# Optimization experiments

Hardware: AMD Instinct MI355X
Metric: run time of the kernel (lower is better)

Reference implementation:

```python
import jax, jax.numpy as jnp
import numpy as np

N = 16      # hparams.length (utterances)
T = 128     # tokens per utterance
D = 256     # local_feature_dim
DG = 256    # global_attention.input_dim
ATT = 128   # attention inner dim
R1 = 2 * N * N  # rgcn num_relations
H1 = 256    # rgcn.dim
H2 = 256    # gcn.dim
NEG = -1e9


def setup_inputs() -> dict:
    ks = jax.random.split(jax.random.key(0), 16)
    s = 0.02
    return {
        "global_features": jax.random.normal(ks[0], (N, DG), jnp.float32),
        "local_features": jax.random.normal(ks[1], (N, T, D), jnp.float32),
        "speaker": jax.random.randint(ks[2], (N,), 0, 2),
        "length": jax.random.randint(ks[3], (N,), 1, T + 1),
        # Bahdanau global attention params
        "Wq": jax.random.normal(ks[4], (DG, ATT), jnp.float32) * s,
        "Wk": jax.random.normal(ks[5], (DG, ATT), jnp.float32) * s,
        "v_att": jax.random.normal(ks[6], (ATT,), jnp.float32) * s,
        # Bidirectional local attention params
        "Wb1": jax.random.normal(ks[7], (D, ATT), jnp.float32) * s,
        "Wb2": jax.random.normal(ks[8], (D, ATT), jnp.float32) * s,
        # RGCN layer 1 (2*N^2 relations)
        "Wrel1": jax.random.normal(ks[9], (R1, D, H1), jnp.float32) * s,
        "Wroot1": jax.random.normal(ks[10], (D, H1), jnp.float32) * s,
        "b1": jnp.zeros((H1,), jnp.float32),
        # RGCN layer 2 (1 relation)
        "Wrel2": jax.random.normal(ks[11], (1, H1, H2), jnp.float32) * s,
        "Wroot2": jax.random.normal(ks[12], (H1, H2), jnp.float32) * s,
        "b2": jnp.zeros((H2,), jnp.float32),
    }


def _rgcn_fg(x, Wrel, Wroot, b, e_src, e_dst, rel, ew, n_nodes):
    # x: [N,T,din], ew: [E,Ts,Td] (src-token x dst-token weights), Wrel: [R,din,dout]
    We = Wrel[rel]                 # [E,din,dout] irregular gather over relations
    xs = x[e_src]                  # [E,T,din]
    # message aligned with dst tokens: sum over src tokens t -> dst token s
    msg = jnp.einsum('ets,etd,edo->eso', ew, xs, We)   # [E,T,dout]
    agg = jax.ops.segment_sum(msg, e_dst, num_segments=n_nodes)
    return agg + x @ Wroot + b


def reference(global_features, local_features, speaker, length,
              Wq, Wk, v_att, Wb1, Wb2,
              Wrel1, Wroot1, b1, Wrel2, Wroot2, b2):
    n = global_features.shape[0]
    t = local_features.shape[1]

    # --- Bahdanau global attention: query i over keys j ---
    q = global_features @ Wq                         # [N,A]
    k = global_features @ Wk                         # [N,A]
    s = jnp.tanh(q[:, None, :] + k[None, :, :]) @ v_att   # [N,N]
    gw = jax.nn.softmax(s, axis=1).reshape(-1)       # [N*N]

    # --- Bidirectional local attention, vectorized over all (i,j) pairs ---
    p1 = local_features @ Wb1                        # [N,T,A]
    p2 = local_features @ Wb2                        # [N,T,A]
    S = jnp.einsum('ita,jsa->ijts', p1, p2)          # [N,N,T,T]
    pos = jnp.arange(t)
    valid = pos[None, :] < length[:, None]           # [N,T]
    S = jnp.where(valid[None, :, None, :], S, NEG)   # mask key tokens of j
    w1 = jax.nn.softmax(S, axis=-1)                  # softmax over j's tokens
    w1 = w1 * valid[:, None, :, None]                # zero padded query rows of i
    lw = w1.reshape(n * n, t, t)                     # [E,T,T]

    # --- edge weights & relation ids ---
    ew1 = gw[:, None, None] * lw                     # [E,T,T]
    e_src = jnp.arange(n * n) // n                   # edge (i,j): src=i
    e_dst = jnp.arange(n * n) % n                    # dst=j
    direction = jnp.where(e_src < e_dst, 0, 1)
    rel = (speaker[e_src] * n + speaker[e_dst]) * 2 + direction

    # --- two attention-weighted relational GCN layers ---
    x1 = _rgcn_fg(local_features, Wrel1, Wroot1, b1, e_src, e_dst, rel, ew1, n)
    x2 = _rgcn_fg(x1, Wrel2, Wroot2, b2, e_src, e_dst, jnp.zeros_like(rel), lw, n)
    return x2
```

## Files before the change

### kernel.cpp

```cpp
#include <hip/hip_runtime.h>

#define NODES 16
#define TT    128
#define DIM   256
#define ATTD  128
#define HD    256
#define NEGV  -1e9f

typedef short bf16x8 __attribute__((ext_vector_type(8)));
typedef float f32x4  __attribute__((ext_vector_type(4)));
typedef unsigned short ushort_t;
typedef ushort_t u16x4 __attribute__((ext_vector_type(4)));
typedef ushort_t u16x8 __attribute__((ext_vector_type(8)));

__device__ __forceinline__ ushort_t f2b(float f) {
  union { float f; unsigned u; } v; v.f = f;
  unsigned r = (v.u + 0x7fffu + ((v.u >> 16) & 1u)) >> 16;
  return (ushort_t)r;
}
__device__ __forceinline__ float b2f(ushort_t h) {
  union { unsigned u; float f; } v; v.u = ((unsigned)h) << 16; return v.f;
}

__device__ __forceinline__ void wave_gemm_step(const ushort_t* __restrict__ A, int as, int R0,
                                               const ushort_t* __restrict__ BT, int bs, int C0,
                                               int kb, int lr, f32x4 acc[4][4]) {
  bf16x8 a[4], b[4];
#pragma unroll
  for (int m = 0; m < 4; ++m)
    a[m] = *(const bf16x8*)(A + (size_t)(R0 + m * 16 + lr) * as + kb);
#pragma unroll
  for (int n = 0; n < 4; ++n)
    b[n] = *(const bf16x8*)(BT + (size_t)(C0 + n * 16 + lr) * bs + kb);
#pragma unroll
  for (int m = 0; m < 4; ++m)
#pragma unroll
    for (int n = 0; n < 4; ++n)
      acc[m][n] = __builtin_amdgcn_mfma_f32_16x16x32_bf16(a[m], b[n], acc[m][n], 0, 0, 0);
}

#define WAVE_SETUP                                    \
  int tid = threadIdx.x;                              \
  int wave = tid >> 6, lane = tid & 63;               \
  int wr = wave >> 1, wc = wave & 1;                  \
  int lr = lane & 15, kg = lane >> 4;                 \
  (void)wr; (void)wc;

#define ACC_INIT(acc)                                 \
  f32x4 acc[4][4];                                    \
  { f32x4 z = {0.f, 0.f, 0.f, 0.f};                   \
    _Pragma("unroll") for (int m = 0; m < 4; ++m)     \
    _Pragma("unroll") for (int n = 0; n < 4; ++n) acc[m][n] = z; }

__device__ __forceinline__ void stage_half(const ushort_t* __restrict__ src, int srcs,
                                           ushort_t* __restrict__ dst, int tid) {
#pragma unroll
  for (int p = 0; p < 4; ++p) {
    int idx = p * 256 + tid;
    int row = idx >> 3;
    int cb  = (idx & 7) << 4;
    u16x8 v = *(const u16x8*)(src + (size_t)row * srcs + (cb >> 1));
    *(u16x8*)((char*)dst + row * 128 + (cb ^ ((row & 7) << 4))) = v;
  }
}

__device__ __forceinline__ void gemm_half(const ushort_t* __restrict__ bufA,
                                          const ushort_t* __restrict__ bufB,
                                          int R0, int C0, int lr, int kg,
                                          f32x4 acc[4][4]) {
#pragma unroll
  for (int kk = 0; kk < 2; ++kk) {
    int cb = kk * 64 + kg * 16;
    bf16x8 a[4], b[4];
#pragma unroll
    for (int m = 0; m < 4; ++m) {
      int row = R0 + m * 16 + lr;
      a[m] = *(const bf16x8*)((const char*)bufA + row * 128 + (cb ^ ((row & 7) << 4)));
    }
#pragma unroll
    for (int n = 0; n < 4; ++n) {
      int row = C0 + n * 16 + lr;
      b[n] = *(const bf16x8*)((const char*)bufB + row * 128 + (cb ^ ((row & 7) << 4)));
    }
#pragma unroll
    for (int m = 0; m < 4; ++m)
#pragma unroll
      for (int n = 0; n < 4; ++n)
        acc[m][n] = __builtin_amdgcn_mfma_f32_16x16x32_bf16(a[m], b[n], acc[m][n], 0, 0, 0);
  }
}

__global__ void k_prep(const float* __restrict__ Lf, ushort_t* __restrict__ Lfh,
                       const float* __restrict__ Wb1, const float* __restrict__ Wb2,
                       const float* __restrict__ Wroot1, const float* __restrict__ Wroot2,
                       const float* __restrict__ Wrel2, const float* __restrict__ Wrel1,
                       ushort_t* __restrict__ Wb1T, ushort_t* __restrict__ Wb2T,
                       ushort_t* __restrict__ Wroot1T, ushort_t* __restrict__ Wroot2T,
                       ushort_t* __restrict__ Wrel2T, ushort_t* __restrict__ Wrel1T8,
                       const float* __restrict__ G, const float* __restrict__ Wq,
                       const float* __restrict__ Wk, float* __restrict__ qk) {
  int blk = blockIdx.x;
  if (blk < 256) {
    int gi = blk * 256 + threadIdx.x;
    const float4* src = (const float4*)Lf;
    float4 v0 = src[gi * 2], v1 = src[gi * 2 + 1];
    u16x8 o;
    o[0] = f2b(v0.x); o[1] = f2b(v0.y); o[2] = f2b(v0.z); o[3] = f2b(v0.w);
    o[4] = f2b(v1.x); o[5] = f2b(v1.y); o[6] = f2b(v1.z); o[7] = f2b(v1.w);
    *(u16x8*)(Lfh + (size_t)gi * 8) = o;
  } else if (blk < 448) {
    __shared__ float lds[64][65];
    int b = blk - 256;
    const float* src; ushort_t* dst; int C, t;
    if (b < 8)       { src = Wb1;    dst = Wb1T;    C = 128; t = b; }
    else if (b < 16) { src = Wb2;    dst = Wb2T;    C = 128; t = b - 8; }
    else if (b < 32) { src = Wroot1; dst = Wroot1T; C = 256; t = b - 16; }
    else if (b < 48) { src = Wroot2; dst = Wroot2T; C = 256; t = b - 32; }
    else if (b < 64) { src = Wrel2;  dst = Wrel2T;  C = 256; t = b - 48; }
    else {
      int m = (b - 64) >> 4;
      int relid = (m >> 2) * 32 + (m & 3);
      src = Wrel1 + (size_t)relid * 65536;
      dst = Wrel1T8 + (size_t)m * 65536;
      C = 256; t = (b - 64) & 15;
    }
    int tilesC = C >> 6;
    int r0 = (t / tilesC) * 64, c0 = (t % tilesC) * 64;
    int tid = threadIdx.x;
    for (int p = 0; p < 16; ++p) {
      int idx = p * 256 + tid, rr = idx >> 6, cc = idx & 63;
      lds[rr][cc] = src[(size_t)(r0 + rr) * C + c0 + cc];
    }
    __syncthreads();
    for (int p = 0; p < 16; ++p) {
      int idx = p * 256 + tid, rr = idx >> 6, cc = idx & 63;
      dst[(size_t)(c0 + rr) * 256 + r0 + cc] = f2b(lds[cc][rr]);
    }
  } else {
    int i = blk - 448, t = threadIdx.x;
    const float* W = (t < 128) ? Wq : Wk;
    int a = t & 127;
    float acc = 0.f;
#pragma unroll 8
    for (int d = 0; d < DIM; ++d)
      acc = fmaf(G[i * DIM + d], W[d * ATTD + a], acc);
    int dst = (t < 128) ? i : (NODES + i);
    qk[(size_t)dst * ATTD + a] = acc;
  }
}

__global__ __launch_bounds__(256, 1)
void k_phaseB(const float* __restrict__ qk, const float* __restrict__ vatt,
              float* __restrict__ gw,
              const ushort_t* __restrict__ Lfh,
              const ushort_t* __restrict__ Wb1T, const ushort_t* __restrict__ Wb2T,
              ushort_t* __restrict__ p1h, ushort_t* __restrict__ p2h,
              const ushort_t* __restrict__ Wroot1T, const float* __restrict__ b1,
              float* __restrict__ x1part,
              const ushort_t* __restrict__ Wrel1T8, const int* __restrict__ spk,
              ushort_t* __restrict__ YT) {
  __shared__ union {
    ushort_t buf[2][16384];
    struct { float sred[NODES][17]; float q[ATTD]; } sc;
  } sh;
  int blk = blockIdx.x;
  if (blk < 16) {
    int i = blk, t = threadIdx.x;
    int j = t >> 4, ag = t & 15;
    if (t < ATTD) sh.sc.q[t] = qk[(size_t)i * ATTD + t];
    __syncthreads();
    float sum = 0.f;
#pragma unroll
    for (int u = 0; u < 8; ++u) {
      int a = ag * 8 + u;
      sum += tanhf(sh.sc.q[a] + qk[(size_t)(NODES + j) * ATTD + a]) * vatt[a];
    }
    sh.sc.sred[j][ag] = sum;
    __syncthreads();
    if (t < NODES) {
      float s = 0.f;
#pragma unroll
      for (int u = 0; u < 16; ++u) s += sh.sc.sred[t][u];
      sh.sc.sred[t][16] = s;
    }
    __syncthreads();
    if (t == 0) {
      float m = -1e30f;
      for (int jj = 0; jj < NODES; ++jj) m = fmaxf(m, sh.sc.sred[jj][16]);
      float ex[NODES], ssum = 0.f;
      for (int jj = 0; jj < NODES; ++jj) { ex[jj] = __expf(sh.sc.sred[jj][16] - m); ssum += ex[jj]; }
      float inv = 1.f / ssum;
      for (int jj = 0; jj < NODES; ++jj) gw[i * NODES + jj] = ex[jj] * inv;
    }
    return;
  }
  WAVE_SETUP
  const ushort_t* Asrc; const ushort_t* Bsrc;
  if (blk < 48) {
    int t = blk - 16; int sel = t >> 4, bx = t & 15;
    Asrc = Lfh + (size_t)bx * 128 * DIM;
    Bsrc = sel ? Wb2T : Wb1T;
  } else if (blk < 80) {
    int t = blk - 48; int bx = t & 15, by = t >> 4;
    Asrc = Lfh + (size_t)bx * 128 * DIM;
    Bsrc = Wroot1T + (size_t)by * 128 * DIM;
  } else {
    int t = blk - 80; int iq = t >> 1, cy = t & 1;
    int i = iq >> 2, q = iq & 3;
    int m8 = spk[i] * 4 + q;
    Asrc = Lfh + (size_t)i * TT * DIM;
    Bsrc = Wrel1T8 + (size_t)m8 * 65536 + (size_t)cy * 128 * DIM;
  }
  stage_half(Asrc, DIM, sh.buf[0], tid);
  stage_half(Bsrc, DIM, sh.buf[0] + 8192, tid);
  __syncthreads();
  ACC_INIT(acc)
  for (int c = 1; c < 4; ++c) {
    stage_half(Asrc + c * 64, DIM, sh.buf[c & 1], tid);
    stage_half(Bsrc + c * 64, DIM, sh.buf[c & 1] + 8192, tid);
    gemm_half(sh.buf[(c & 1) ^ 1], sh.buf[(c & 1) ^ 1] + 8192, wr * 64, wc * 64, lr, kg, acc);
    __syncthreads();
  }
  gemm_half(sh.buf[1], sh.buf[1] + 8192, wr * 64, wc * 64, lr, kg, acc);
  if (blk < 48) {
    int t = blk - 16; int sel = t >> 4, bx = t & 15;
    ushort_t* out = sel ? p2h : p1h;
    int R0 = bx * 128 + wr * 64, C0 = wc * 64;
#pragma unroll
    for (int m = 0; m < 4; ++m)
#pragma unroll
      for (int n = 0; n < 4; ++n) {
        int col = C0 + n * 16 + lr;
#pragma unroll
        for (int r = 0; r < 4; ++r) {
          int row = R0 + m * 16 + kg * 4 + r;
          out[(size_t)row * ATTD + col] = f2b(acc[m][n][r]);
        }
      }
  } else if (blk < 80) {
    int t = blk - 48; int bx = t & 15, by = t >> 4;
    int R0 = bx * 128 + wr * 64, C0 = by * 128 + wc * 64;
#pragma unroll
    for (int m = 0; m < 4; ++m)
#pragma unroll
      for (int n = 0; n < 4; ++n) {
        int col = C0 + n * 16 + lr;
        float bb = b1[col];
#pragma unroll
        for (int r = 0; r < 4; ++r) {
          int row = R0 + m * 16 + kg * 4 + r;
          x1part[(size_t)row * HD + col] = acc[m][n][r] + bb;
        }
      }
  } else {
    int t = blk - 80; int iq = t >> 1, cy = t & 1;
    int R0 = wr * 64, C0 = cy * 128 + wc * 64;
#pragma unroll
    for (int m = 0; m < 4; ++m)
#pragma unroll
      for (int n = 0; n < 4; ++n) {
        int o = C0 + n * 16 + lr;
        int t0 = R0 + m * 16 + kg * 4;
        u16x4 v;
#pragma unroll
        for (int r = 0; r < 4; ++r) v[r] = f2b(acc[m][n][r]);
        *(u16x4*)(YT + (size_t)iq * 32768 + (size_t)o * TT + t0) = v;
      }
  }
}

__global__ __launch_bounds__(256, 1)
void k_locatt(const ushort_t* __restrict__ p1h, const ushort_t* __restrict__ p2h,
              const int* __restrict__ length,
              ushort_t* __restrict__ lwT) {
  __shared__ union {
    ushort_t buf[2][16384];
    float S[TT][129];
  } sh;
  __shared__ float red[TT][2];
  __shared__ float sInv[TT];
  int e = blockIdx.x, i = e >> 4, j = e & 15;
  WAVE_SETUP
  int R0 = wr * 64, C0 = wc * 64;
  const ushort_t* A = p1h + (size_t)i * TT * ATTD;
  const ushort_t* B = p2h + (size_t)j * TT * ATTD;
  stage_half(A, ATTD, sh.buf[0], tid);
  stage_half(B, ATTD, sh.buf[0] + 8192, tid);
  __syncthreads();
  stage_half(A + 64, ATTD, sh.buf[1], tid);
  stage_half(B + 64, ATTD, sh.buf[1] + 8192, tid);
  ACC_INIT(acc)
  gemm_half(sh.buf[0], sh.buf[0] + 8192, R0, C0, lr, kg, acc);
  __syncthreads();
  gemm_half(sh.buf[1], sh.buf[1] + 8192, R0, C0, lr, kg, acc);
  __syncthreads();
#pragma unroll
  for (int m = 0; m < 4; ++m)
#pragma unroll
    for (int n = 0; n < 4; ++n)
#pragma unroll
      for (int r = 0; r < 4; ++r)
        sh.S[R0 + m * 16 + kg * 4 + r][C0 + n * 16 + lr] = acc[m][n][r];
  __syncthreads();
  int leni = length[i], lenj = length[j];
  int t = tid & 127, h = tid >> 7, s0 = h * 64;
  float mx = -1e30f;
  for (int s = s0; s < s0 + 64; ++s) {
    float vv = (s < lenj) ? sh.S[t][s] : NEGV;
    mx = fmaxf(mx, vv);
  }
  red[t][h] = mx;
  __syncthreads();
  mx = fmaxf(red[t][0], red[t][1]);
  __syncthreads();
  float sum = 0.f;
  for (int s = s0; s < s0 + 64; ++s) {
    float vv = (s < lenj) ? sh.S[t][s] : NEGV;
    float ee = __expf(vv - mx);
    sh.S[t][s] = ee;
    sum += ee;
  }
  red[t][h] = sum;
  __syncthreads();
  if (h == 0) sInv[t] = (t < leni) ? 1.f / (red[t][0] + red[t][1]) : 0.f;
  __syncthreads();
  int s = tid >> 1;
  int t0 = (tid & 1) * 64;
  size_t base = (size_t)e * 16384 + (size_t)s * TT;
  for (int tb = 0; tb < 64; tb += 8) {
    u16x8 w;
#pragma unroll
    for (int u = 0; u < 8; ++u) {
      int tt = t0 + tb + u;
      w[u] = f2b(sh.S[tt][s] * sInv[tt]);
    }
    *(u16x8*)(lwT + base + t0 + tb) = w;
  }
}

__global__ __launch_bounds__(256, 1)
void k_wagg(const ushort_t* __restrict__ lwT, const ushort_t* __restrict__ Bsrc,
            const float* __restrict__ gw, const int* __restrict__ spk,
            ushort_t* __restrict__ partH, int mode) {
  __shared__ ushort_t buf[2][16384];
  int g = blockIdx.x, j = blockIdx.y, oh = blockIdx.z;
  WAVE_SETUP
  int R0 = wr * 64, C0 = wc * 64;
  int i0 = g * 2, i1 = g * 2 + 1;
  int e0 = i0 * NODES + j, e1 = i1 * NODES + j;
  const ushort_t* B0;
  const ushort_t* B1;
  float ge0, ge1;
  if (mode == 1) {
    int q0 = spk[j] * 2 + ((i0 < j) ? 0 : 1);
    int q1 = spk[j] * 2 + ((i1 < j) ? 0 : 1);
    B0 = Bsrc + (size_t)(i0 * 4 + q0) * 32768 + (size_t)oh * 16384;
    B1 = Bsrc + (size_t)(i1 * 4 + q1) * 32768 + (size_t)oh * 16384;
    ge0 = gw[e0]; ge1 = gw[e1];
  } else {
    B0 = Bsrc + (size_t)i0 * 32768 + (size_t)oh * 16384;
    B1 = Bsrc + (size_t)i1 * 32768 + (size_t)oh * 16384;
    ge0 = 1.f; ge1 = 1.f;
  }
  const ushort_t* A0 = lwT + (size_t)e0 * 16384;
  const ushort_t* A1 = lwT + (size_t)e1 * 16384;
  stage_half(A0, TT, buf[0], tid);
  stage_half(B0, TT, buf[0] + 8192, tid);
  __syncthreads();
  stage_half(A0 + 64, TT, buf[1], tid);
  stage_half(B0 + 64, TT, buf[1] + 8192, tid);
  ACC_INIT(acc0)
  gemm_half(buf[0], buf[0] + 8192, R0, C0, lr, kg, acc0);
  __syncthreads();
  stage_half(A1, TT, buf[0], tid);
  stage_half(B1, TT, buf[0] + 8192, tid);
  gemm_half(buf[1], buf[1] + 8192, R0, C0, lr, kg, acc0);
  __syncthreads();
  stage_half(A1 + 64, TT, buf[1], tid);
  stage_half(B1 + 64, TT, buf[1] + 8192, tid);
  ACC_INIT(acc1)
  gemm_half(buf[0], buf[0] + 8192, R0, C0, lr, kg, acc1);
  __syncthreads();
  gemm_half(buf[1], buf[1] + 8192, R0, C0, lr, kg, acc1);
  size_t base = (size_t)(g * NODES + j) * TT * HD + (size_t)oh * 128;
#pragma unroll
  for (int m = 0; m < 4; ++m)
#pragma unroll
    for (int n = 0; n < 4; ++n) {
      int ocol = C0 + n * 16 + lr;
#pragma unroll
      for (int r = 0; r < 4; ++r) {
        int s = R0 + m * 16 + kg * 4 + r;
        partH[base + (size_t)s * HD + ocol] = f2b(ge0 * acc0[m][n][r] + ge1 * acc1[m][n][r]);
      }
    }
}

__global__ __launch_bounds__(256, 1)
void k_reduce1(const ushort_t* __restrict__ partH, const float* __restrict__ x1part,
               ushort_t* __restrict__ x1h, ushort_t* __restrict__ x1T) {
  __shared__ ushort_t L[TT][40];
  int j = blockIdx.x, oc0 = blockIdx.y * 32, tid = threadIdx.x;
  const size_t Q = (size_t)NODES * TT * HD;
#pragma unroll
  for (int p = 0; p < 4; ++p) {
    int idx = p * 256 + tid;
    int t = idx >> 3, o4 = (idx & 7) * 4;
    size_t goff = ((size_t)j * TT + t) * HD + oc0 + o4;
    float4 s = *(const float4*)(x1part + goff);
#pragma unroll
    for (int g = 0; g < 8; ++g) {
      u16x4 pv = *(const u16x4*)(partH + (size_t)g * Q + goff);
      s.x += b2f(pv[0]); s.y += b2f(pv[1]); s.z += b2f(pv[2]); s.w += b2f(pv[3]);
    }
    u16x4 hv; hv[0] = f2b(s.x); hv[1] = f2b(s.y); hv[2] = f2b(s.z); hv[3] = f2b(s.w);
    *(u16x4*)(x1h + goff) = hv;
    *(u16x4*)(&L[t][o4]) = hv;
  }
  __syncthreads();
#pragma unroll
  for (int p = 0; p < 2; ++p) {
    int idx = p * 256 + tid;
    int o = idx >> 4, t8 = (idx & 15) * 8;
    u16x8 v;
#pragma unroll
    for (int u = 0; u < 8; ++u) v[u] = L[t8 + u][o];
    *(u16x8*)(x1T + (size_t)j * 32768 + (size_t)(oc0 + o) * TT + t8) = v;
  }
}

__global__ void k_reduce2(const ushort_t* __restrict__ partH, ushort_t* __restrict__ Z2h) {
  int idx = blockIdx.x * 256 + threadIdx.x;
  size_t o4 = (size_t)idx * 4;
  const size_t Q = (size_t)NODES * TT * HD;
  float4 s = {0.f, 0.f, 0.f, 0.f};
#pragma unroll
  for (int g = 0; g < 8; ++g) {
    u16x4 pv = *(const u16x4*)(partH + (size_t)g * Q + o4);
    s.x += b2f(pv[0]); s.y += b2f(pv[1]); s.z += b2f(pv[2]); s.w += b2f(pv[3]);
  }
  u16x4 hv; hv[0] = f2b(s.x); hv[1] = f2b(s.y); hv[2] = f2b(s.z); hv[3] = f2b(s.w);
  *(u16x4*)(Z2h + o4) = hv;
}

__global__ __launch_bounds__(64, 1)
void k_final(const ushort_t* __restrict__ Z2h, const ushort_t* __restrict__ Wrel2T,
             const ushort_t* __restrict__ x1h, const ushort_t* __restrict__ Wroot2T,
             const float* __restrict__ b2, float* __restrict__ out) {
  int lane = threadIdx.x;
  int lr = lane & 15, kg = lane >> 4;
  int R0 = blockIdx.x * 64, C0 = blockIdx.y * 32;
  f32x4 acc[4][2];
  { f32x4 z = {0.f, 0.f, 0.f, 0.f};
#pragma unroll
    for (int m = 0; m < 4; ++m)
#pragma unroll
      for (int n = 0; n < 2; ++n) acc[m][n] = z; }
  for (int src = 0; src < 2; ++src) {
    const ushort_t* A  = src ? x1h : Z2h;
    const ushort_t* BT = src ? Wroot2T : Wrel2T;
    for (int kk = 0; kk < 8; ++kk) {
      int kb = kk * 32 + kg * 8;
      bf16x8 a[4], b[2];
#pragma unroll
      for (int m = 0; m < 4; ++m)
        a[m] = *(const bf16x8*)(A + (size_t)(R0 + m * 16 + lr) * HD + kb);
#pragma unroll
      for (int n = 0; n < 2; ++n)
        b[n] = *(const bf16x8*)(BT + (size_t)(C0 + n * 16 + lr) * HD + kb);
#pragma unroll
      for (int m = 0; m < 4; ++m)
#pragma unroll
        for (int n = 0; n < 2; ++n)
          acc[m][n] = __builtin_amdgcn_mfma_f32_16x16x32_bf16(a[m], b[n], acc[m][n], 0, 0, 0);
    }
  }
#pragma unroll
  for (int m = 0; m < 4; ++m)
#pragma unroll
    for (int n = 0; n < 2; ++n) {
      int col = C0 + n * 16 + lr;
      float bb = b2[col];
#pragma unroll
      for (int r = 0; r < 4; ++r) {
        int row = R0 + m * 16 + kg * 4 + r;
        out[(size_t)row * HD + col] = acc[m][n][r] + bb;
      }
    }
}

extern "C" void kernel_launch(void* const* d_in, const int* in_sizes, int n_in,
                              void* d_out, int out_size, void* d_ws, size_t ws_size,
                              hipStream_t stream) {
  (void)in_sizes; (void)n_in; (void)out_size; (void)ws_size;
  const float* G      = (const float*)d_in[0];
  const float* Lf     = (const float*)d_in[1];
  const int*   spk    = (const int*)d_in[2];
  const int*   len    = (const int*)d_in[3];
  const float* Wq     = (const float*)d_in[4];
  const float* Wk     = (const float*)d_in[5];
  const float* vatt   = (const float*)d_in[6];
  const float* Wb1    = (const float*)d_in[7];
  const float* Wb2    = (const float*)d_in[8];
  const float* Wrel1  = (const float*)d_in[9];
  const float* Wroot1 = (const float*)d_in[10];
  const float* b1     = (const float*)d_in[11];
  const float* Wrel2  = (const float*)d_in[12];
  const float* Wroot2 = (const float*)d_in[13];
  const float* b2     = (const float*)d_in[14];

  char* ws = (char*)d_ws;
  const size_t MB = 1ull << 20;
  float*    gw      = (float*)(ws);
  float*    qk      = (float*)(ws + 16 * 1024);
  ushort_t* Lfh     = (ushort_t*)(ws + 1 * MB);
  ushort_t* Wb1T    = (ushort_t*)(ws + 2 * MB);
  ushort_t* Wb2T    = (ushort_t*)(ws + 2 * MB + 64 * 1024);
  ushort_t* Wroot1T = (ushort_t*)(ws + 2 * MB + 128 * 1024);
  ushort_t* Wroot2T = (ushort_t*)(ws + 2 * MB + 256 * 1024);
  ushort_t* Wrel2T  = (ushort_t*)(ws + 2 * MB + 384 * 1024);
  ushort_t* Wrel1T8 = (ushort_t*)(ws + 2 * MB + 512 * 1024);
  ushort_t* p1h     = (ushort_t*)(ws + 4 * MB);
  ushort_t* p2h     = (ushort_t*)(ws + 4 * MB + 512 * 1024);
  ushort_t* lwT     = (ushort_t*)(ws + 5 * MB);
  ushort_t* YT      = (ushort_t*)(ws + 21 * MB);
  float*    x1part  = (float*)(ws + 25 * MB);
  ushort_t* partH   = (ushort_t*)(ws + 27 * MB);
  ushort_t* x1h     = (ushort_t*)(ws + 43 * MB);
  ushort_t* x1T     = (ushort_t*)(ws + 44 * MB);
  ushort_t* Z2h     = (ushort_t*)(ws + 45 * MB);
  float* out = (float*)d_out;

  k_prep<<<464, 256, 0, stream>>>(Lf, Lfh, Wb1, Wb2, Wroot1, Wroot2, Wrel2, Wrel1,
                                  Wb1T, Wb2T, Wroot1T, Wroot2T, Wrel2T, Wrel1T8,
                                  G, Wq, Wk, qk);
  k_phaseB<<<208, 256, 0, stream>>>(qk, vatt, gw, Lfh, Wb1T, Wb2T, p1h, p2h,
                                    Wroot1T, b1, x1part, Wrel1T8, spk, YT);
  k_locatt<<<256, 256, 0, stream>>>(p1h, p2h, len, lwT);
  k_wagg<<<dim3(8, 16, 2), 256, 0, stream>>>(lwT, YT, gw, spk, partH, 1);
  k_reduce1<<<dim3(16, 8), 256, 0, stream>>>(partH, x1part, x1h, x1T);
  k_wagg<<<dim3(8, 16, 2), 256, 0, stream>>>(lwT, x1T, gw, spk, partH, 2);
  k_reduce2<<<512, 256, 0, stream>>>(partH, Z2h);
  k_final<<<dim3(32, 8), 64, 0, stream>>>(Z2h, Wrel2T, x1h, Wroot2T, b2, out);
}
```

Measured before the change: 73.54 us.

## Fuse all stages into one persistent megakernel with atomic grid barriers

Replaces the eight separate kernel launches with a single persistent kernel of 256 blocks. Each former kernel becomes a phase, and phases are separated by software grid barriers built on atomic counters, which are zeroed by a memset before the launch. This is meant to remove the per-launch overhead and the tail gaps between the small dependent kernels. The cost is spin-wait barriers that assume all 256 blocks are resident at once, load imbalance inside each phase, and one shared-memory union sized for the largest phase.

```diff
diff --git a/kernel.cpp b/kernel.cpp
--- a/kernel.cpp
+++ b/kernel.cpp
@@ -6,6 +6,7 @@
 #define ATTD  128
 #define HD    256
 #define NEGV  -1e9f
+#define NBLK  256
 
 typedef short bf16x8 __attribute__((ext_vector_type(8)));
 typedef float f32x4  __attribute__((ext_vector_type(4)));
@@ -22,6 +23,19 @@
   union { unsigned u; float f; } v; v.u = ((unsigned)h) << 16; return v.f;
 }
 
+__device__ __forceinline__ void gbar(unsigned* __restrict__ ctr, int idx) {
+  __syncthreads();
+  if (threadIdx.x == 0) {
+    __threadfence();
+    atomicAdd(&ctr[idx], 1u);
+    while (__hip_atomic_load(&ctr[idx], __ATOMIC_RELAXED,
+                             __HIP_MEMORY_SCOPE_AGENT) < (unsigned)NBLK)
+      __builtin_amdgcn_s_sleep(8);
+    __threadfence();
+  }
+  __syncthreads();
+}
+
 __device__ __forceinline__ void wave_gemm_step(const ushort_t* __restrict__ A, int as, int R0,
                                                const ushort_t* __restrict__ BT, int bs, int C0,
                                                int kb, int lr, f32x4 acc[4][4]) {
@@ -38,13 +52,6 @@
     for (int n = 0; n < 4; ++n)
       acc[m][n] = __builtin_amdgcn_mfma_f32_16x16x32_bf16(a[m], b[n], acc[m][n], 0, 0, 0);
 }
-
-#define WAVE_SETUP                                    \
-  int tid = threadIdx.x;                              \
-  int wave = tid >> 6, lane = tid & 63;               \
-  int wr = wave >> 1, wc = wave & 1;                  \
-  int lr = lane & 15, kg = lane >> 4;                 \
-  (void)wr; (void)wc;
 
 #define ACC_INIT(acc)                                 \
   f32x4 acc[4][4];                                    \
@@ -90,266 +97,36 @@
   }
 }
 
-__global__ void k_prep(const float* __restrict__ Lf, ushort_t* __restrict__ Lfh,
-                       const float* __restrict__ Wb1, const float* __restrict__ Wb2,
-                       const float* __restrict__ Wroot1, const float* __restrict__ Wroot2,
-                       const float* __restrict__ Wrel2, const float* __restrict__ Wrel1,
-                       ushort_t* __restrict__ Wb1T, ushort_t* __restrict__ Wb2T,
-                       ushort_t* __restrict__ Wroot1T, ushort_t* __restrict__ Wroot2T,
-                       ushort_t* __restrict__ Wrel2T, ushort_t* __restrict__ Wrel1T8,
-                       const float* __restrict__ G, const float* __restrict__ Wq,
-                       const float* __restrict__ Wk, float* __restrict__ qk) {
-  int blk = blockIdx.x;
-  if (blk < 256) {
-    int gi = blk * 256 + threadIdx.x;
-    const float4* src = (const float4*)Lf;
-    float4 v0 = src[gi * 2], v1 = src[gi * 2 + 1];
-    u16x8 o;
-    o[0] = f2b(v0.x); o[1] = f2b(v0.y); o[2] = f2b(v0.z); o[3] = f2b(v0.w);
-    o[4] = f2b(v1.x); o[5] = f2b(v1.y); o[6] = f2b(v1.z); o[7] = f2b(v1.w);
-    *(u16x8*)(Lfh + (size_t)gi * 8) = o;
-  } else if (blk < 448) {
-    __shared__ float lds[64][65];
-    int b = blk - 256;
-    const float* src; ushort_t* dst; int C, t;
-    if (b < 8)       { src = Wb1;    dst = Wb1T;    C = 128; t = b; }
-    else if (b < 16) { src = Wb2;    dst = Wb2T;    C = 128; t = b - 8; }
-    else if (b < 32) { src = Wroot1; dst = Wroot1T; C = 256; t = b - 16; }
-    else if (b < 48) { src = Wroot2; dst = Wroot2T; C = 256; t = b - 32; }
-    else if (b < 64) { src = Wrel2;  dst = Wrel2T;  C = 256; t = b - 48; }
-    else {
-      int m = (b - 64) >> 4;
-      int relid = (m >> 2) * 32 + (m & 3);
-      src = Wrel1 + (size_t)relid * 65536;
-      dst = Wrel1T8 + (size_t)m * 65536;
-      C = 256; t = (b - 64) & 15;
-    }
-    int tilesC = C >> 6;
-    int r0 = (t / tilesC) * 64, c0 = (t % tilesC) * 64;
-    int tid = threadIdx.x;
-    for (int p = 0; p < 16; ++p) {
-      int idx = p * 256 + tid, rr = idx >> 6, cc = idx & 63;
-      lds[rr][cc] = src[(size_t)(r0 + rr) * C + c0 + cc];
-    }
-    __syncthreads();
-    for (int p = 0; p < 16; ++p) {
-      int idx = p * 256 + tid, rr = idx >> 6, cc = idx & 63;
-      dst[(size_t)(c0 + rr) * 256 + r0 + cc] = f2b(lds[cc][rr]);
-    }
-  } else {
-    int i = blk - 448, t = threadIdx.x;
-    const float* W = (t < 128) ? Wq : Wk;
-    int a = t & 127;
-    float acc = 0.f;
-#pragma unroll 8
-    for (int d = 0; d < DIM; ++d)
-      acc = fmaf(G[i * DIM + d], W[d * ATTD + a], acc);
-    int dst = (t < 128) ? i : (NODES + i);
-    qk[(size_t)dst * ATTD + a] = acc;
-  }
-}
-
-__global__ __launch_bounds__(256, 1)
-void k_phaseB(const float* __restrict__ qk, const float* __restrict__ vatt,
-              float* __restrict__ gw,
-              const ushort_t* __restrict__ Lfh,
-              const ushort_t* __restrict__ Wb1T, const ushort_t* __restrict__ Wb2T,
-              ushort_t* __restrict__ p1h, ushort_t* __restrict__ p2h,
-              const ushort_t* __restrict__ Wroot1T, const float* __restrict__ b1,
-              float* __restrict__ x1part,
-              const ushort_t* __restrict__ Wrel1T8, const int* __restrict__ spk,
-              ushort_t* __restrict__ YT) {
-  __shared__ union {
-    ushort_t buf[2][16384];
-    struct { float sred[NODES][17]; float q[ATTD]; } sc;
-  } sh;
-  int blk = blockIdx.x;
-  if (blk < 16) {
-    int i = blk, t = threadIdx.x;
-    int j = t >> 4, ag = t & 15;
-    if (t < ATTD) sh.sc.q[t] = qk[(size_t)i * ATTD + t];
-    __syncthreads();
-    float sum = 0.f;
-#pragma unroll
-    for (int u = 0; u < 8; ++u) {
-      int a = ag * 8 + u;
-      sum += tanhf(sh.sc.q[a] + qk[(size_t)(NODES + j) * ATTD + a]) * vatt[a];
-    }
-    sh.sc.sred[j][ag] = sum;
-    __syncthreads();
-    if (t < NODES) {
-      float s = 0.f;
-#pragma unroll
-      for (int u = 0; u < 16; ++u) s += sh.sc.sred[t][u];
-      sh.sc.sred[t][16] = s;
-    }
-    __syncthreads();
-    if (t == 0) {
-      float m = -1e30f;
-      for (int jj = 0; jj < NODES; ++jj) m = fmaxf(m, sh.sc.sred[jj][16]);
-      float ex[NODES], ssum = 0.f;
-      for (int jj = 0; jj < NODES; ++jj) { ex[jj] = __expf(sh.sc.sred[jj][16] - m); ssum += ex[jj]; }
-      float inv = 1.f / ssum;
-      for (int jj = 0; jj < NODES; ++jj) gw[i * NODES + jj] = ex[jj] * inv;
-    }
-    return;
-  }
-  WAVE_SETUP
-  const ushort_t* Asrc; const ushort_t* Bsrc;
-  if (blk < 48) {
-    int t = blk - 16; int sel = t >> 4, bx = t & 15;
-    Asrc = Lfh + (size_t)bx * 128 * DIM;
-    Bsrc = sel ? Wb2T : Wb1T;
-  } else if (blk < 80) {
-    int t = blk - 48; int bx = t & 15, by = t >> 4;
-    Asrc = Lfh + (size_t)bx * 128 * DIM;
-    Bsrc = Wroot1T + (size_t)by * 128 * DIM;
-  } else {
-    int t = blk - 80; int iq = t >> 1, cy = t & 1;
-    int i = iq >> 2, q = iq & 3;
-    int m8 = spk[i] * 4 + q;
-    Asrc = Lfh + (size_t)i * TT * DIM;
-    Bsrc = Wrel1T8 + (size_t)m8 * 65536 + (size_t)cy * 128 * DIM;
-  }
-  stage_half(Asrc, DIM, sh.buf[0], tid);
-  stage_half(Bsrc, DIM, sh.buf[0] + 8192, tid);
-  __syncthreads();
-  ACC_INIT(acc)
-  for (int c = 1; c < 4; ++c) {
-    stage_half(Asrc + c * 64, DIM, sh.buf[c & 1], tid);
-    stage_half(Bsrc + c * 64, DIM, sh.buf[c & 1] + 8192, tid);
-    gemm_half(sh.buf[(c & 1) ^ 1], sh.buf[(c & 1) ^ 1] + 8192, wr * 64, wc * 64, lr, kg, acc);
-    __syncthreads();
-  }
-  gemm_half(sh.buf[1], sh.buf[1] + 8192, wr * 64, wc * 64, lr, kg, acc);
-  if (blk < 48) {
-    int t = blk - 16; int sel = t >> 4, bx = t & 15;
-    ushort_t* out = sel ? p2h : p1h;
-    int R0 = bx * 128 + wr * 64, C0 = wc * 64;
-#pragma unroll
-    for (int m = 0; m < 4; ++m)
-#pragma unroll
-      for (int n = 0; n < 4; ++n) {
-        int col = C0 + n * 16 + lr;
-#pragma unroll
-        for (int r = 0; r < 4; ++r) {
-          int row = R0 + m * 16 + kg * 4 + r;
-          out[(size_t)row * ATTD + col] = f2b(acc[m][n][r]);
-        }
-      }
-  } else if (blk < 80) {
-    int t = blk - 48; int bx = t & 15, by = t >> 4;
-    int R0 = bx * 128 + wr * 64, C0 = by * 128 + wc * 64;
-#pragma unroll
-    for (int m = 0; m < 4; ++m)
-#pragma unroll
-      for (int n = 0; n < 4; ++n) {
-        int col = C0 + n * 16 + lr;
-        float bb = b1[col];
-#pragma unroll
-        for (int r = 0; r < 4; ++r) {
-          int row = R0 + m * 16 + kg * 4 + r;
-          x1part[(size_t)row * HD + col] = acc[m][n][r] + bb;
-        }
-      }
-  } else {
-    int t = blk - 80; int iq = t >> 1, cy = t & 1;
-    int R0 = wr * 64, C0 = cy * 128 + wc * 64;
-#pragma unroll
-    for (int m = 0; m < 4; ++m)
-#pragma unroll
-      for (int n = 0; n < 4; ++n) {
-        int o = C0 + n * 16 + lr;
-        int t0 = R0 + m * 16 + kg * 4;
-        u16x4 v;
-#pragma unroll
-        for (int r = 0; r < 4; ++r) v[r] = f2b(acc[m][n][r]);
-        *(u16x4*)(YT + (size_t)iq * 32768 + (size_t)o * TT + t0) = v;
-      }
-  }
-}
-
-__global__ __launch_bounds__(256, 1)
-void k_locatt(const ushort_t* __restrict__ p1h, const ushort_t* __restrict__ p2h,
-              const int* __restrict__ length,
-              ushort_t* __restrict__ lwT) {
-  __shared__ union {
-    ushort_t buf[2][16384];
-    float S[TT][129];
-  } sh;
-  __shared__ float red[TT][2];
-  __shared__ float sInv[TT];
-  int e = blockIdx.x, i = e >> 4, j = e & 15;
-  WAVE_SETUP
-  int R0 = wr * 64, C0 = wc * 64;
-  const ushort_t* A = p1h + (size_t)i * TT * ATTD;
-  const ushort_t* B = p2h + (size_t)j * TT * ATTD;
-  stage_half(A, ATTD, sh.buf[0], tid);
-  stage_half(B, ATTD, sh.buf[0] + 8192, tid);
-  __syncthreads();
-  stage_half(A + 64, ATTD, sh.buf[1], tid);
-  stage_half(B + 64, ATTD, sh.buf[1] + 8192, tid);
-  ACC_INIT(acc)
-  gemm_half(sh.buf[0], sh.buf[0] + 8192, R0, C0, lr, kg, acc);
-  __syncthreads();
-  gemm_half(sh.buf[1], sh.buf[1] + 8192, R0, C0, lr, kg, acc);
-  __syncthreads();
-#pragma unroll
-  for (int m = 0; m < 4; ++m)
-#pragma unroll
-    for (int n = 0; n < 4; ++n)
-#pragma unroll
-      for (int r = 0; r < 4; ++r)
-        sh.S[R0 + m * 16 + kg * 4 + r][C0 + n * 16 + lr] = acc[m][n][r];
-  __syncthreads();
-  int leni = length[i], lenj = length[j];
-  int t = tid & 127, h = tid >> 7, s0 = h * 64;
-  float mx = -1e30f;
-  for (int s = s0; s < s0 + 64; ++s) {
-    float vv = (s < lenj) ? sh.S[t][s] : NEGV;
-    mx = fmaxf(mx, vv);
-  }
-  red[t][h] = mx;
-  __syncthreads();
-  mx = fmaxf(red[t][0], red[t][1]);
-  __syncthreads();
-  float sum = 0.f;
-  for (int s = s0; s < s0 + 64; ++s) {
-    float vv = (s < lenj) ? sh.S[t][s] : NEGV;
-    float ee = __expf(vv - mx);
-    sh.S[t][s] = ee;
-    sum += ee;
-  }
-  red[t][h] = sum;
-  __syncthreads();
-  if (h == 0) sInv[t] = (t < leni) ? 1.f / (red[t][0] + red[t][1]) : 0.f;
-  __syncthreads();
-  int s = tid >> 1;
-  int t0 = (tid & 1) * 64;
-  size_t base = (size_t)e * 16384 + (size_t)s * TT;
-  for (int tb = 0; tb < 64; tb += 8) {
-    u16x8 w;
-#pragma unroll
-    for (int u = 0; u < 8; ++u) {
-      int tt = t0 + tb + u;
-      w[u] = f2b(sh.S[tt][s] * sInv[tt]);
-    }
-    *(u16x8*)(lwT + base + t0 + tb) = w;
-  }
-}
-
-__global__ __launch_bounds__(256, 1)
-void k_wagg(const ushort_t* __restrict__ lwT, const ushort_t* __restrict__ Bsrc,
-            const float* __restrict__ gw, const int* __restrict__ spk,
-            ushort_t* __restrict__ partH, int mode) {
-  __shared__ ushort_t buf[2][16384];
-  int g = blockIdx.x, j = blockIdx.y, oh = blockIdx.z;
-  WAVE_SETUP
+struct MegaParams {
+  const float *Lf, *Wb1, *Wb2, *Wroot1, *Wroot2, *Wrel2, *Wrel1;
+  const float *G, *Wq, *Wk, *vatt, *b1, *b2;
+  const int *spk, *len;
+  ushort_t *Lfh, *Wb1T, *Wb2T, *Wroot1T, *Wroot2T, *Wrel2T, *Wrel1T8;
+  ushort_t *p1h, *p2h, *lwT, *YT, *x1h, *x1T, *Z2h, *partH;
+  float *gw, *qk, *x1part, *out;
+  unsigned *ctr;
+};
+
+union ShMem {
+  ushort_t buf[2][16384];
+  float S[TT][129];
+  float tr[64][65];
+  struct { float sred[NODES][17]; float q[ATTD]; } sc;
+  ushort_t L[TT][40];
+};
+
+__device__ __forceinline__ void wagg_phase(int bid, int tid, int wr, int wc,
+                                           int lr, int kg, ShMem& sh,
+                                           const ushort_t* __restrict__ lwT,
+                                           const ushort_t* __restrict__ Bsrc,
+                                           const float* __restrict__ gw,
+                                           const int* __restrict__ spk,
+                                           ushort_t* __restrict__ partH, int mode) {
+  int g = bid >> 5, j = (bid >> 1) & 15, oh = bid & 1;
   int R0 = wr * 64, C0 = wc * 64;
   int i0 = g * 2, i1 = g * 2 + 1;
   int e0 = i0 * NODES + j, e1 = i1 * NODES + j;
-  const ushort_t* B0;
-  const ushort_t* B1;
+  const ushort_t *B0, *B1;
   float ge0, ge1;
   if (mode == 1) {
     int q0 = spk[j] * 2 + ((i0 < j) ? 0 : 1);
@@ -364,24 +141,24 @@
   }
   const ushort_t* A0 = lwT + (size_t)e0 * 16384;
   const ushort_t* A1 = lwT + (size_t)e1 * 16384;
-  stage_half(A0, TT, buf[0], tid);
-  stage_half(B0, TT, buf[0] + 8192, tid);
+  stage_half(A0, TT, sh.buf[0], tid);
+  stage_half(B0, TT, sh.buf[0] + 8192, tid);
   __syncthreads();
-  stage_half(A0 + 64, TT, buf[1], tid);
-  stage_half(B0 + 64, TT, buf[1] + 8192, tid);
+  stage_half(A0 + 64, TT, sh.buf[1], tid);
+  stage_half(B0 + 64, TT, sh.buf[1] + 8192, tid);
   ACC_INIT(acc0)
-  gemm_half(buf[0], buf[0] + 8192, R0, C0, lr, kg, acc0);
+  gemm_half(sh.buf[0], sh.buf[0] + 8192, R0, C0, lr, kg, acc0);
   __syncthreads();
-  stage_half(A1, TT, buf[0], tid);
-  stage_half(B1, TT, buf[0] + 8192, tid);
-  gemm_half(buf[1], buf[1] + 8192, R0, C0, lr, kg, acc0);
+  stage_half(A1, TT, sh.buf[0], tid);
+  stage_half(B1, TT, sh.buf[0] + 8192, tid);
+  gemm_half(sh.buf[1], sh.buf[1] + 8192, R0, C0, lr, kg, acc0);
   __syncthreads();
-  stage_half(A1 + 64, TT, buf[1], tid);
-  stage_half(B1 + 64, TT, buf[1] + 8192, tid);
+  stage_half(A1 + 64, TT, sh.buf[1], tid);
+  stage_half(B1 + 64, TT, sh.buf[1] + 8192, tid);
   ACC_INIT(acc1)
-  gemm_half(buf[0], buf[0] + 8192, R0, C0, lr, kg, acc1);
+  gemm_half(sh.buf[0], sh.buf[0] + 8192, R0, C0, lr, kg, acc1);
   __syncthreads();
-  gemm_half(buf[1], buf[1] + 8192, R0, C0, lr, kg, acc1);
+  gemm_half(sh.buf[1], sh.buf[1] + 8192, R0, C0, lr, kg, acc1);
   size_t base = (size_t)(g * NODES + j) * TT * HD + (size_t)oh * 128;
 #pragma unroll
   for (int m = 0; m < 4; ++m)
@@ -397,149 +174,368 @@
 }
 
 __global__ __launch_bounds__(256, 1)
-void k_reduce1(const ushort_t* __restrict__ partH, const float* __restrict__ x1part,
-               ushort_t* __restrict__ x1h, ushort_t* __restrict__ x1T) {
-  __shared__ ushort_t L[TT][40];
-  int j = blockIdx.x, oc0 = blockIdx.y * 32, tid = threadIdx.x;
+void k_mega(MegaParams P) {
+  __shared__ ShMem sh;
+  __shared__ float red[TT][2];
+  __shared__ float sInv[TT];
+  const int bid = blockIdx.x;
+  const int tid = threadIdx.x;
+  const int wave = tid >> 6, lane = tid & 63;
+  const int wr = wave >> 1, wc = wave & 1;
+  const int lr = lane & 15, kg = lane >> 4;
   const size_t Q = (size_t)NODES * TT * HD;
-#pragma unroll
-  for (int p = 0; p < 4; ++p) {
-    int idx = p * 256 + tid;
-    int t = idx >> 3, o4 = (idx & 7) * 4;
-    size_t goff = ((size_t)j * TT + t) * HD + oc0 + o4;
-    float4 s = *(const float4*)(x1part + goff);
+
+  {
+    int gi = bid * 256 + tid;
+    const float4* src = (const float4*)P.Lf;
+    float4 v0 = src[gi * 2], v1 = src[gi * 2 + 1];
+    u16x8 o;
+    o[0] = f2b(v0.x); o[1] = f2b(v0.y); o[2] = f2b(v0.z); o[3] = f2b(v0.w);
+    o[4] = f2b(v1.x); o[5] = f2b(v1.y); o[6] = f2b(v1.z); o[7] = f2b(v1.w);
+    *(u16x8*)(P.Lfh + (size_t)gi * 8) = o;
+  }
+  if (bid < 192) {
+    int b = bid;
+    const float* src; ushort_t* dst; int C, t;
+    if (b < 8)       { src = P.Wb1;    dst = P.Wb1T;    C = 128; t = b; }
+    else if (b < 16) { src = P.Wb2;    dst = P.Wb2T;    C = 128; t = b - 8; }
+    else if (b < 32) { src = P.Wroot1; dst = P.Wroot1T; C = 256; t = b - 16; }
+    else if (b < 48) { src = P.Wroot2; dst = P.Wroot2T; C = 256; t = b - 32; }
+    else if (b < 64) { src = P.Wrel2;  dst = P.Wrel2T;  C = 256; t = b - 48; }
+    else {
+      int m = (b - 64) >> 4;
+      int relid = (m >> 2) * 32 + (m & 3);
+      src = P.Wrel1 + (size_t)relid * 65536;
+      dst = P.Wrel1T8 + (size_t)m * 65536;
+      C = 256; t = (b - 64) & 15;
+    }
+    int tilesC = C >> 6;
+    int r0 = (t / tilesC) * 64, c0 = (t % tilesC) * 64;
+    for (int p = 0; p < 16; ++p) {
+      int idx = p * 256 + tid, rr = idx >> 6, cc = idx & 63;
+      sh.tr[rr][cc] = src[(size_t)(r0 + rr) * C + c0 + cc];
+    }
+    __syncthreads();
+    for (int p = 0; p < 16; ++p) {
+      int idx = p * 256 + tid, rr = idx >> 6, cc = idx & 63;
+      dst[(size_t)(c0 + rr) * 256 + r0 + cc] = f2b(sh.tr[cc][rr]);
+    }
+  } else if (bid < 208) {
+    int i = bid - 192;
+    const float* W = (tid < 128) ? P.Wq : P.Wk;
+    int a = tid & 127;
+    float acc = 0.f;
+#pragma unroll 8
+    for (int d = 0; d < DIM; ++d)
+      acc = fmaf(P.G[i * DIM + d], W[d * ATTD + a], acc);
+    int dst = (tid < 128) ? i : (NODES + i);
+    P.qk[(size_t)dst * ATTD + a] = acc;
+  }
+  gbar(P.ctr, 0);
+
+  if (bid < 16) {
+    int i = bid;
+    int j = tid >> 4, ag = tid & 15;
+    if (tid < ATTD) sh.sc.q[tid] = P.qk[(size_t)i * ATTD + tid];
+    __syncthreads();
+    float sum = 0.f;
+#pragma unroll
+    for (int u = 0; u < 8; ++u) {
+      int a = ag * 8 + u;
+      sum += tanhf(sh.sc.q[a] + P.qk[(size_t)(NODES + j) * ATTD + a]) * P.vatt[a];
+    }
+    sh.sc.sred[j][ag] = sum;
+    __syncthreads();
+    if (tid < NODES) {
+      float s = 0.f;
+#pragma unroll
+      for (int u = 0; u < 16; ++u) s += sh.sc.sred[tid][u];
+      sh.sc.sred[tid][16] = s;
+    }
+    __syncthreads();
+    if (tid == 0) {
+      float m = -1e30f;
+      for (int jj = 0; jj < NODES; ++jj) m = fmaxf(m, sh.sc.sred[jj][16]);
+      float ex[NODES], ssum = 0.f;
+      for (int jj = 0; jj < NODES; ++jj) { ex[jj] = __expf(sh.sc.sred[jj][16] - m); ssum += ex[jj]; }
+      float inv = 1.f / ssum;
+      for (int jj = 0; jj < NODES; ++jj) P.gw[i * NODES + jj] = ex[jj] * inv;
+    }
+  } else if (bid < 208) {
+    const ushort_t *Asrc, *Bsrc;
+    if (bid < 48) {
+      int t = bid - 16; int sel = t >> 4, bx = t & 15;
+      Asrc = P.Lfh + (size_t)bx * 128 * DIM;
+      Bsrc = sel ? P.Wb2T : P.Wb1T;
+    } else if (bid < 80) {
+      int t = bid - 48; int bx = t & 15, by = t >> 4;
+      Asrc = P.Lfh + (size_t)bx * 128 * DIM;
+      Bsrc = P.Wroot1T + (size_t)by * 128 * DIM;
+    } else {
+      int t = bid - 80; int iq = t >> 1, cy = t & 1;
+      int i = iq >> 2, q = iq & 3;
+      int m8 = P.spk[i] * 4 + q;
+      Asrc = P.Lfh + (size_t)i * TT * DIM;
+      Bsrc = P.Wrel1T8 + (size_t)m8 * 65536 + (size_t)cy * 128 * DIM;
+    }
+    stage_half(Asrc, DIM, sh.buf[0], tid);
+    stage_half(Bsrc, DIM, sh.buf[0] + 8192, tid);
+    __syncthreads();
+    ACC_INIT(acc)
+    for (int c = 1; c < 4; ++c) {
+      stage_half(Asrc + c * 64, DIM, sh.buf[c & 1], tid);
+      stage_half(Bsrc + c * 64, DIM, sh.buf[c & 1] + 8192, tid);
+      gemm_half(sh.buf[(c & 1) ^ 1], sh.buf[(c & 1) ^ 1] + 8192, wr * 64, wc * 64, lr, kg, acc);
+      __syncthreads();
+    }
+    gemm_half(sh.buf[1], sh.buf[1] + 8192, wr * 64, wc * 64, lr, kg, acc);
+    if (bid < 48) {
+      int t = bid - 16; int sel = t >> 4, bx = t & 15;
+      ushort_t* out = sel ? P.p2h : P.p1h;
+      int R0 = bx * 128 + wr * 64, C0 = wc * 64;
+#pragma unroll
+      for (int m = 0; m < 4; ++m)
+#pragma unroll
+        for (int n = 0; n < 4; ++n) {
+          int col = C0 + n * 16 + lr;
+#pragma unroll
+          for (int r = 0; r < 4; ++r) {
+            int row = R0 + m * 16 + kg * 4 + r;
+            out[(size_t)row * ATTD + col] = f2b(acc[m][n][r]);
+          }
+        }
+    } else if (bid < 80) {
+      int t = bid - 48; int bx = t & 15, by = t >> 4;
+      int R0 = bx * 128 + wr * 64, C0 = by * 128 + wc * 64;
+#pragma unroll
+      for (int m = 0; m < 4; ++m)
+#pragma unroll
+        for (int n = 0; n < 4; ++n) {
+          int col = C0 + n * 16 + lr;
+          float bb = P.b1[col];
+#pragma unroll
+          for (int r = 0; r < 4; ++r) {
+            int row = R0 + m * 16 + kg * 4 + r;
+            P.x1part[(size_t)row * HD + col] = acc[m][n][r] + bb;
+          }
+        }
+    } else {
+      int t = bid - 80; int iq = t >> 1, cy = t & 1;
+      int R0 = wr * 64, C0 = cy * 128 + wc * 64;
+#pragma unroll
+      for (int m = 0; m < 4; ++m)
+#pragma unroll
+        for (int n = 0; n < 4; ++n) {
+          int o = C0 + n * 16 + lr;
+          int t0 = R0 + m * 16 + kg * 4;
+          u16x4 v;
+#pragma unroll
+          for (int r = 0; r < 4; ++r) v[r] = f2b(acc[m][n][r]);
+          *(u16x4*)(P.YT + (size_t)iq * 32768 + (size_t)o * TT + t0) = v;
+        }
+    }
+  }
+  gbar(P.ctr, 1);
+
+  {
+    int e = bid, i = e >> 4, j = e & 15;
+    int R0 = wr * 64, C0 = wc * 64;
+    const ushort_t* A = P.p1h + (size_t)i * TT * ATTD;
+    const ushort_t* B = P.p2h + (size_t)j * TT * ATTD;
+    stage_half(A, ATTD, sh.buf[0], tid);
+    stage_half(B, ATTD, sh.buf[0] + 8192, tid);
+    __syncthreads();
+    stage_half(A + 64, ATTD, sh.buf[1], tid);
+    stage_half(B + 64, ATTD, sh.buf[1] + 8192, tid);
+    ACC_INIT(acc)
+    gemm_half(sh.buf[0], sh.buf[0] + 8192, R0, C0, lr, kg, acc);
+    __syncthreads();
+    gemm_half(sh.buf[1], sh.buf[1] + 8192, R0, C0, lr, kg, acc);
+    __syncthreads();
+#pragma unroll
+    for (int m = 0; m < 4; ++m)
+#pragma unroll
+      for (int n = 0; n < 4; ++n)
+#pragma unroll
+        for (int r = 0; r < 4; ++r)
+          sh.S[R0 + m * 16 + kg * 4 + r][C0 + n * 16 + lr] = acc[m][n][r];
+    __syncthreads();
+    int leni = P.len[i], lenj = P.len[j];
+    int t = tid & 127, h = tid >> 7, s0 = h * 64;
+    float mx = -1e30f;
+    for (int s = s0; s < s0 + 64; ++s) {
+      float vv = (s < lenj) ? sh.S[t][s] : NEGV;
+      mx = fmaxf(mx, vv);
+    }
+    red[t][h] = mx;
+    __syncthreads();
+    mx = fmaxf(red[t][0], red[t][1]);
+    __syncthreads();
+    float sum = 0.f;
+    for (int s = s0; s < s0 + 64; ++s) {
+      float vv = (s < lenj) ? sh.S[t][s] : NEGV;
+      float ee = __expf(vv - mx);
+      sh.S[t][s] = ee;
+      sum += ee;
+    }
+    red[t][h] = sum;
+    __syncthreads();
+    if (h == 0) sInv[t] = (t < leni) ? 1.f / (red[t][0] + red[t][1]) : 0.f;
+    __syncthreads();
+    int s = tid >> 1;
+    int t0 = (tid & 1) * 64;
+    size_t base = (size_t)e * 16384 + (size_t)s * TT;
+    for (int tb = 0; tb < 64; tb += 8) {
+      u16x8 w;
+#pragma unroll
+      for (int u = 0; u < 8; ++u) {
+        int tt = t0 + tb + u;
+        w[u] = f2b(sh.S[tt][s] * sInv[tt]);
+      }
+      *(u16x8*)(P.lwT + base + t0 + tb) = w;
+    }
+  }
+  gbar(P.ctr, 2);
+
+  wagg_phase(bid, tid, wr, wc, lr, kg, sh, P.lwT, P.YT, P.gw, P.spk, P.partH, 1);
+  gbar(P.ctr, 3);
+
+  if (bid < 128) {
+    int j = bid >> 3, oc0 = (bid & 7) * 32;
+#pragma unroll
+    for (int p = 0; p < 4; ++p) {
+      int idx = p * 256 + tid;
+      int t = idx >> 3, o4 = (idx & 7) * 4;
+      size_t goff = ((size_t)j * TT + t) * HD + oc0 + o4;
+      float4 s = *(const float4*)(P.x1part + goff);
+#pragma unroll
+      for (int g = 0; g < 8; ++g) {
+        u16x4 pv = *(const u16x4*)(P.partH + (size_t)g * Q + goff);
+        s.x += b2f(pv[0]); s.y += b2f(pv[1]); s.z += b2f(pv[2]); s.w += b2f(pv[3]);
+      }
+      u16x4 hv; hv[0] = f2b(s.x); hv[1] = f2b(s.y); hv[2] = f2b(s.z); hv[3] = f2b(s.w);
+      *(u16x4*)(P.x1h + goff) = hv;
+      *(u16x4*)(&sh.L[t][o4]) = hv;
+    }
+    __syncthreads();
+#pragma unroll
+    for (int p = 0; p < 2; ++p) {
+      int idx = p * 256 + tid;
+      int o = idx >> 4, t8 = (idx & 15) * 8;
+      u16x8 v;
+#pragma unroll
+      for (int u = 0; u < 8; ++u) v[u] = sh.L[t8 + u][o];
+      *(u16x8*)(P.x1T + (size_t)j * 32768 + (size_t)(oc0 + o) * TT + t8) = v;
+    }
+  }
+  gbar(P.ctr, 4);
+
+  wagg_phase(bid, tid, wr, wc, lr, kg, sh, P.lwT, P.x1T, P.gw, P.spk, P.partH, 2);
+  gbar(P.ctr, 5);
+
+#pragma unroll
+  for (int pass = 0; pass < 2; ++pass) {
+    int idx = (pass * 256 + bid) * 256 + tid;
+    size_t o4 = (size_t)idx * 4;
+    float4 s = {0.f, 0.f, 0.f, 0.f};
 #pragma unroll
     for (int g = 0; g < 8; ++g) {
-      u16x4 pv = *(const u16x4*)(partH + (size_t)g * Q + goff);
+      u16x4 pv = *(const u16x4*)(P.partH + (size_t)g * Q + o4);
       s.x += b2f(pv[0]); s.y += b2f(pv[1]); s.z += b2f(pv[2]); s.w += b2f(pv[3]);
     }
     u16x4 hv; hv[0] = f2b(s.x); hv[1] = f2b(s.y); hv[2] = f2b(s.z); hv[3] = f2b(s.w);
-    *(u16x4*)(x1h + goff) = hv;
-    *(u16x4*)(&L[t][o4]) = hv;
-  }
-  __syncthreads();
-#pragma unroll
-  for (int p = 0; p < 2; ++p) {
-    int idx = p * 256 + tid;
-    int o = idx >> 4, t8 = (idx & 15) * 8;
-    u16x8 v;
-#pragma unroll
-    for (int u = 0; u < 8; ++u) v[u] = L[t8 + u][o];
-    *(u16x8*)(x1T + (size_t)j * 32768 + (size_t)(oc0 + o) * TT + t8) = v;
-  }
-}
-
-__global__ void k_reduce2(const ushort_t* __restrict__ partH, ushort_t* __restrict__ Z2h) {
-  int idx = blockIdx.x * 256 + threadIdx.x;
-  size_t o4 = (size_t)idx * 4;
-  const size_t Q = (size_t)NODES * TT * HD;
-  float4 s = {0.f, 0.f, 0.f, 0.f};
-#pragma unroll
-  for (int g = 0; g < 8; ++g) {
-    u16x4 pv = *(const u16x4*)(partH + (size_t)g * Q + o4);
-    s.x += b2f(pv[0]); s.y += b2f(pv[1]); s.z += b2f(pv[2]); s.w += b2f(pv[3]);
-  }
-  u16x4 hv; hv[0] = f2b(s.x); hv[1] = f2b(s.y); hv[2] = f2b(s.z); hv[3] = f2b(s.w);
-  *(u16x4*)(Z2h + o4) = hv;
-}
-
-__global__ __launch_bounds__(64, 1)
-void k_final(const ushort_t* __restrict__ Z2h, const ushort_t* __restrict__ Wrel2T,
-             const ushort_t* __restrict__ x1h, const ushort_t* __restrict__ Wroot2T,
-             const float* __restrict__ b2, float* __restrict__ out) {
-  int lane = threadIdx.x;
-  int lr = lane & 15, kg = lane >> 4;
-  int R0 = blockIdx.x * 64, C0 = blockIdx.y * 32;
-  f32x4 acc[4][2];
-  { f32x4 z = {0.f, 0.f, 0.f, 0.f};
+    *(u16x4*)(P.Z2h + o4) = hv;
+  }
+  gbar(P.ctr, 6);
+
+  if (bid < 64) {
+    int R0 = (bid & 31) * 64;
+    int C0 = (bid >> 5) * 128 + wave * 32;
+    f32x4 acc[4][2];
+    { f32x4 z = {0.f, 0.f, 0.f, 0.f};
+#pragma unroll
+      for (int m = 0; m < 4; ++m)
+#pragma unroll
+        for (int n = 0; n < 2; ++n) acc[m][n] = z; }
+    for (int src = 0; src < 2; ++src) {
+      const ushort_t* A  = src ? P.x1h : P.Z2h;
+      const ushort_t* BT = src ? P.Wroot2T : P.Wrel2T;
+      for (int kk = 0; kk < 8; ++kk) {
+        int kb = kk * 32 + kg * 8;
+        bf16x8 a[4], b[2];
+#pragma unroll
+        for (int m = 0; m < 4; ++m)
+          a[m] = *(const bf16x8*)(A + (size_t)(R0 + m * 16 + lr) * HD + kb);
+#pragma unroll
+        for (int n = 0; n < 2; ++n)
+          b[n] = *(const bf16x8*)(BT + (size_t)(C0 + n * 16 + lr) * HD + kb);
+#pragma unroll
+        for (int m = 0; m < 4; ++m)
+#pragma unroll
+          for (int n = 0; n < 2; ++n)
+            acc[m][n] = __builtin_amdgcn_mfma_f32_16x16x32_bf16(a[m], b[n], acc[m][n], 0, 0, 0);
+      }
+    }
 #pragma unroll
     for (int m = 0; m < 4; ++m)
 #pragma unroll
-      for (int n = 0; n < 2; ++n) acc[m][n] = z; }
-  for (int src = 0; src < 2; ++src) {
-    const ushort_t* A  = src ? x1h : Z2h;
-    const ushort_t* BT = src ? Wroot2T : Wrel2T;
-    for (int kk = 0; kk < 8; ++kk) {
-      int kb = kk * 32 + kg * 8;
-      bf16x8 a[4], b[2];
-#pragma unroll
-      for (int m = 0; m < 4; ++m)
-        a[m] = *(const bf16x8*)(A + (size_t)(R0 + m * 16 + lr) * HD + kb);
-#pragma unroll
-      for (int n = 0; n < 2; ++n)
-        b[n] = *(const bf16x8*)(BT + (size_t)(C0 + n * 16 + lr) * HD + kb);
-#pragma unroll
-      for (int m = 0; m < 4; ++m)
-#pragma unroll
-        for (int n = 0; n < 2; ++n)
-          acc[m][n] = __builtin_amdgcn_mfma_f32_16x16x32_bf16(a[m], b[n], acc[m][n], 0, 0, 0);
-    }
-  }
-#pragma unroll
-  for (int m = 0; m < 4; ++m)
-#pragma unroll
-    for (int n = 0; n < 2; ++n) {
-      int col = C0 + n * 16 + lr;
-      float bb = b2[col];
-#pragma unroll
-      for (int r = 0; r < 4; ++r) {
-        int row = R0 + m * 16 + kg * 4 + r;
-        out[(size_t)row * HD + col] = acc[m][n][r] + bb;
+      for (int n = 0; n < 2; ++n) {
+        int col = C0 + n * 16 + lr;
+        float bb = P.b2[col];
+#pragma unroll
+        for (int r = 0; r < 4; ++r) {
+          int row = R0 + m * 16 + kg * 4 + r;
+          P.out[(size_t)row * HD + col] = acc[m][n][r] + bb;
+        }
       }
-    }
+  }
 }
 
 extern "C" void kernel_launch(void* const* d_in, const int* in_sizes, int n_in,
                               void* d_out, int out_size, void* d_ws, size_t ws_size,
                               hipStream_t stream) {
   (void)in_sizes; (void)n_in; (void)out_size; (void)ws_size;
-  const float* G      = (const float*)d_in[0];
-  const float* Lf     = (const float*)d_in[1];
-  const int*   spk    = (const int*)d_in[2];
-  const int*   len    = (const int*)d_in[3];
-  const float* Wq     = (const float*)d_in[4];
-  const float* Wk     = (const float*)d_in[5];
-  const float* vatt   = (const float*)d_in[6];
-  const float* Wb1    = (const float*)d_in[7];
-  const float* Wb2    = (const float*)d_in[8];
-  const float* Wrel1  = (const float*)d_in[9];
-  const float* Wroot1 = (const float*)d_in[10];
-  const float* b1     = (const float*)d_in[11];
-  const float* Wrel2  = (const float*)d_in[12];
-  const float* Wroot2 = (const float*)d_in[13];
-  const float* b2     = (const float*)d_in[14];
-
   char* ws = (char*)d_ws;
   const size_t MB = 1ull << 20;
-  float*    gw      = (float*)(ws);
-  float*    qk      = (float*)(ws + 16 * 1024);
-  ushort_t* Lfh     = (ushort_t*)(ws + 1 * MB);
-  ushort_t* Wb1T    = (ushort_t*)(ws + 2 * MB);
-  ushort_t* Wb2T    = (ushort_t*)(ws + 2 * MB + 64 * 1024);
-  ushort_t* Wroot1T = (ushort_t*)(ws + 2 * MB + 128 * 1024);
-  ushort_t* Wroot2T = (ushort_t*)(ws + 2 * MB + 256 * 1024);
-  ushort_t* Wrel2T  = (ushort_t*)(ws + 2 * MB + 384 * 1024);
-  ushort_t* Wrel1T8 = (ushort_t*)(ws + 2 * MB + 512 * 1024);
-  ushort_t* p1h     = (ushort_t*)(ws + 4 * MB);
-  ushort_t* p2h     = (ushort_t*)(ws + 4 * MB + 512 * 1024);
-  ushort_t* lwT     = (ushort_t*)(ws + 5 * MB);
-  ushort_t* YT      = (ushort_t*)(ws + 21 * MB);
-  float*    x1part  = (float*)(ws + 25 * MB);
-  ushort_t* partH   = (ushort_t*)(ws + 27 * MB);
-  ushort_t* x1h     = (ushort_t*)(ws + 43 * MB);
-  ushort_t* x1T     = (ushort_t*)(ws + 44 * MB);
-  ushort_t* Z2h     = (ushort_t*)(ws + 45 * MB);
-  float* out = (float*)d_out;
-
-  k_prep<<<464, 256, 0, stream>>>(Lf, Lfh, Wb1, Wb2, Wroot1, Wroot2, Wrel2, Wrel1,
-                                  Wb1T, Wb2T, Wroot1T, Wroot2T, Wrel2T, Wrel1T8,
-                                  G, Wq, Wk, qk);
-  k_phaseB<<<208, 256, 0, stream>>>(qk, vatt, gw, Lfh, Wb1T, Wb2T, p1h, p2h,
-                                    Wroot1T, b1, x1part, Wrel1T8, spk, YT);
-  k_locatt<<<256, 256, 0, stream>>>(p1h, p2h, len, lwT);
-  k_wagg<<<dim3(8, 16, 2), 256, 0, stream>>>(lwT, YT, gw, spk, partH, 1);
-  k_reduce1<<<dim3(16, 8), 256, 0, stream>>>(partH, x1part, x1h, x1T);
-  k_wagg<<<dim3(8, 16, 2), 256, 0, stream>>>(lwT, x1T, gw, spk, partH, 2);
-  k_reduce2<<<512, 256, 0, stream>>>(partH, Z2h);
-  k_final<<<dim3(32, 8), 64, 0, stream>>>(Z2h, Wrel2T, x1h, Wroot2T, b2, out);
-}
+
+  MegaParams P;
+  P.G      = (const float*)d_in[0];
+  P.Lf     = (const float*)d_in[1];
+  P.spk    = (const int*)d_in[2];
+  P.len    = (const int*)d_in[3];
+  P.Wq     = (const float*)d_in[4];
+  P.Wk     = (const float*)d_in[5];
+  P.vatt   = (const float*)d_in[6];
+  P.Wb1    = (const float*)d_in[7];
+  P.Wb2    = (const float*)d_in[8];
+  P.Wrel1  = (const float*)d_in[9];
+  P.Wroot1 = (const float*)d_in[10];
+  P.b1     = (const float*)d_in[11];
+  P.Wrel2  = (const float*)d_in[12];
+  P.Wroot2 = (const float*)d_in[13];
+  P.b2     = (const float*)d_in[14];
+
+  P.gw      = (float*)(ws);
+  P.qk      = (float*)(ws + 16 * 1024);
+  P.Lfh     = (ushort_t*)(ws + 1 * MB);
+  P.Wb1T    = (ushort_t*)(ws + 2 * MB);
+  P.Wb2T    = (ushort_t*)(ws + 2 * MB + 64 * 1024);
+  P.Wroot1T = (ushort_t*)(ws + 2 * MB + 128 * 1024);
+  P.Wroot2T = (ushort_t*)(ws + 2 * MB + 256 * 1024);
+  P.Wrel2T  = (ushort_t*)(ws + 2 * MB + 384 * 1024);
+  P.Wrel1T8 = (ushort_t*)(ws + 2 * MB + 512 * 1024);
+  P.p1h     = (ushort_t*)(ws + 4 * MB);
+  P.p2h     = (ushort_t*)(ws + 4 * MB + 512 * 1024);
+  P.lwT     = (ushort_t*)(ws + 5 * MB);
+  P.YT      = (ushort_t*)(ws + 21 * MB);
+  P.x1part  = (float*)(ws + 25 * MB);
+  P.partH   = (ushort_t*)(ws + 27 * MB);
+  P.x1h     = (ushort_t*)(ws + 43 * MB);
+  P.x1T     = (ushort_t*)(ws + 44 * MB);
+  P.Z2h     = (ushort_t*)(ws + 45 * MB);
+  P.ctr     = (unsigned*)(ws + 47 * MB);
+  P.out     = (float*)d_out;
+
+  hipMemsetAsync(P.ctr, 0, 64, stream);
+  k_mega<<<NBLK, 256, 0, stream>>>(P);
+}
```

Result: slower. 240.2 us (+226.7%).
